# Kernel tuning notes

Measured on AMD Instinct MI355X. Metric: run time of the kernel, lower is better.

## Reference

```python
import jax, jax.numpy as jnp
import numpy as np

N = 50000      # nodes
E = 1600000    # edges (avg degree 32)
F_IN = 128     # num_features
DIM = 64       # hidden dim
L = 3          # num_gc_layers
G = 500        # graphs in batch


def setup_inputs() -> dict:
    key = jax.random.key(0)
    ks = jax.random.split(key, 16)
    inp = {}
    inp["x"] = jax.random.normal(ks[0], (N, F_IN), dtype=jnp.float32)
    inp["edge_index"] = jax.random.randint(ks[1], (2, E), 0, N, dtype=jnp.int32)
    inp["batch"] = jnp.sort(jax.random.randint(ks[2], (N,), 0, G, dtype=jnp.int32))
    # GIN layer MLP params: layer0 maps F_IN->DIM->DIM, later layers DIM->DIM->DIM
    d_in = F_IN
    ki = 3
    for i in range(L):
        inp[f"W1_{i}"] = jax.random.normal(ks[ki], (d_in, DIM), dtype=jnp.float32) / np.sqrt(d_in); ki += 1
        inp[f"b1_{i}"] = jnp.zeros((DIM,), dtype=jnp.float32)
        inp[f"W2_{i}"] = jax.random.normal(ks[ki], (DIM, DIM), dtype=jnp.float32) / np.sqrt(DIM); ki += 1
        inp[f"b2_{i}"] = jnp.zeros((DIM,), dtype=jnp.float32)
        d_in = DIM
    # final scoring head: concat readout -> dim * L inputs, 1 output
    inp["Wm"] = jax.random.normal(ks[ki], (DIM * L, 1), dtype=jnp.float32) / np.sqrt(DIM * L)
    inp["bm"] = jnp.zeros((1,), dtype=jnp.float32)
    return inp


def _segment_softmax(scores, seg, num_segments):
    # numerically stable softmax over elements grouped by seg; scores [M, 1]
    m = jax.ops.segment_max(scores, seg, num_segments=num_segments)
    e = jnp.exp(scores - m[seg])
    denom = jax.ops.segment_sum(e, seg, num_segments=num_segments)
    return e / denom[seg]


def _forward(x, edge_index, batch, params):
    src, dst = edge_index[0], edge_index[1]
    n = x.shape[0]
    xs = []
    h = x
    for i in range(L):
        W1, b1, W2, b2 = params[4 * i: 4 * i + 4]
        # GINConv (eps=0): h_i <- MLP(h_i + sum_{j->i} h_j)
        agg = jax.ops.segment_sum(h[src], dst, num_segments=n)
        h = jax.nn.relu((h + agg) @ W1 + b1) @ W2 + b2
        if i != L - 1:
            h = jax.nn.relu(h)
        xs.append(h)
    node_prob = jnp.concatenate(xs, axis=1)            # concat readout [N, DIM*L]
    Wm, bm = params[4 * L], params[4 * L + 1]
    node_score = node_prob @ Wm + bm                   # [N, 1]
    # lift_node_score_to_edge_score
    src_score = node_score[src]                        # [E, 1]
    dst_score = node_score[dst]
    edge_score = src_score * dst_score
    edge_prop = _segment_softmax(edge_score, dst, n)   # softmax over edges per dst
    new_score = jax.ops.segment_sum(src_score * edge_prop, dst, num_segments=n)
    node_score = node_score + new_score
    # final softmax over nodes grouped by graph id
    return _segment_softmax(node_score, batch, G)


def reference(x, edge_index, batch, W1_0, b1_0, W2_0, b2_0, W1_1, b1_1, W2_1, b2_1,
              W1_2, b1_2, W2_2, b2_2, Wm, bm):
    params = [W1_0, b1_0, W2_0, b2_0, W1_1, b1_1, W2_1, b2_1,
              W1_2, b1_2, W2_2, b2_2, Wm, bm]
    return _forward(x, edge_index, batch, params)
```

## Files before the change

### kernel.cpp

```cpp
#include <hip/hip_runtime.h>
#include <hip/hip_fp16.h>
#include <math.h>

#define N_NODES 50000
#define N_EDGES 1600000
#define N_GRAPH 500
#define CHUNKS 128
#define EPC (N_EDGES / CHUNKS)
#define NP1 (N_NODES + 1)
#define NIT ((EPC + 1023) / 1024)

__device__ __forceinline__ float rl(float v, int k) {
    return __int_as_float(__builtin_amdgcn_readlane(__float_as_int(v), k));
}
__device__ __forceinline__ void hacc(float4& a, uint2 w) {
    __half2 h01 = *reinterpret_cast<__half2*>(&w.x);
    __half2 h23 = *reinterpret_cast<__half2*>(&w.y);
    float2 f01 = __half22float2(h01);
    float2 f23 = __half22float2(h23);
    a.x += f01.x; a.y += f01.y; a.z += f23.x; a.w += f23.y;
}

__global__ __launch_bounds__(1024) void histsort_kernel(const int* __restrict__ src,
                                                        const int* __restrict__ dst,
                                                        int* __restrict__ csrc_chunk,
                                                        unsigned short* __restrict__ locs) {
    __shared__ unsigned packed[N_NODES / 2];
    __shared__ unsigned aux[1024];
    const int c = blockIdx.x;
    const int s0 = c * EPC;
    const int tid = threadIdx.x;

    for (int i = tid; i < N_NODES / 2; i += 1024) packed[i] = 0;
    __syncthreads();

    unsigned short lrv[NIT];
#pragma unroll
    for (int it = 0; it < NIT; it++) {
        int e = s0 + it * 1024 + tid;
        if (e < s0 + EPC) {
            int d = dst[e];
            int sh = (d & 1) * 16;
            unsigned old = atomicAdd(&packed[d >> 1], 1u << sh);
            lrv[it] = (unsigned short)((old >> sh) & 0xffffu);
        }
    }
    __syncthreads();

    const int W = 25;
    int w0 = tid * W;
    int w1 = min(w0 + W, N_NODES / 2);
    unsigned run = 0;
    for (int i = w0; i < w1; i++) {
        unsigned v = packed[i];
        unsigned lo = v & 0xffffu, hi = v >> 16;
        packed[i] = run | ((run + lo) << 16);
        run += lo + hi;
    }
    aux[tid] = run;
    __syncthreads();
    for (int off = 1; off < 1024; off <<= 1) {
        unsigned t = (tid >= off) ? aux[tid - off] : 0;
        __syncthreads();
        aux[tid] += t;
        __syncthreads();
    }
    unsigned b0 = (tid == 0) ? 0 : aux[tid - 1];
    if (b0) {
        unsigned addv = b0 | (b0 << 16);
        for (int i = w0; i < w1; i++) packed[i] += addv;
    }
    __syncthreads();

    int* outc = csrc_chunk + (size_t)c * EPC;
#pragma unroll
    for (int it = 0; it < NIT; it++) {
        int e = s0 + it * 1024 + tid;
        if (e < s0 + EPC) {
            int d = dst[e];
            unsigned pw = packed[d >> 1];
            unsigned loc = (d & 1) ? (pw >> 16) : (pw & 0xffffu);
            outc[loc + lrv[it]] = src[e];
        }
    }
    unsigned short* lc = locs + (size_t)c * NP1;
    for (int d = tid; d <= N_NODES; d += 1024) {
        unsigned short loc;
        if (d == N_NODES) {
            loc = (unsigned short)EPC;
        } else {
            unsigned pw = packed[d >> 1];
            loc = (unsigned short)((d & 1) ? (pw >> 16) : (pw & 0xffffu));
        }
        lc[d] = loc;
    }
}

__global__ __launch_bounds__(1024) void base_scan1_kernel(const unsigned short* __restrict__ locs,
                                                          unsigned short* __restrict__ base,
                                                          int* __restrict__ deg,
                                                          int* __restrict__ part, int N) {
    int d = blockIdx.x * 1024 + threadIdx.x;
    int run = 0;
    if (d < N) {
#pragma unroll 8
        for (int c = 0; c < CHUNKS; c++) {
            int l0 = locs[(size_t)c * NP1 + d];
            int l1 = locs[(size_t)c * NP1 + d + 1];
            base[(size_t)c * N + d] = (unsigned short)run;
            run += l1 - l0;
        }
        deg[d] = run;
    }
    int v = run;
#pragma unroll
    for (int o = 32; o >= 1; o >>= 1) v += __shfl_xor(v, o);
    __shared__ int red[16];
    if ((threadIdx.x & 63) == 0) red[threadIdx.x >> 6] = v;
    __syncthreads();
    if (threadIdx.x == 0) {
        int s = 0;
#pragma unroll
        for (int k = 0; k < 16; k++) s += red[k];
        part[blockIdx.x] = s;
    }
}

__global__ void scan2_kernel(int* __restrict__ part, int nb) {
    int lane = threadIdx.x;
    int v = (lane < nb) ? part[lane] : 0;
    int orig = v;
#pragma unroll
    for (int o = 1; o < 64; o <<= 1) {
        int t = __shfl_up(v, o);
        if (lane >= o) v += t;
    }
    if (lane < nb) part[lane] = v - orig;
    if (lane == nb - 1) part[nb] = v;
}

__global__ __launch_bounds__(1024) void scan3_kernel(const int* __restrict__ deg,
                                                     const int* __restrict__ part,
                                                     int* __restrict__ rowptr, int N) {
    int i = blockIdx.x * 1024 + threadIdx.x;
    int lane = threadIdx.x & 63;
    int w = threadIdx.x >> 6;
    int v = (i < N) ? deg[i] : 0;
    int inc = v;
#pragma unroll
    for (int o = 1; o < 64; o <<= 1) {
        int t = __shfl_up(inc, o);
        if (lane >= o) inc += t;
    }
    __shared__ int wsum[16];
    if (lane == 63) wsum[w] = inc;
    __syncthreads();
    if (threadIdx.x < 16) {
        int x = wsum[threadIdx.x];
        int xo = x;
#pragma unroll
        for (int o = 1; o < 16; o <<= 1) {
            int t = __shfl_up(x, o);
            if ((int)threadIdx.x >= o) x += t;
        }
        wsum[threadIdx.x] = x - xo;
    }
    __syncthreads();
    int b = part[blockIdx.x] + wsum[w];
    if (i < N) {
        rowptr[i] = b + inc - v;
        if (i == N - 1) rowptr[N] = b + inc;
    }
}

__global__ __launch_bounds__(256) void gatherfill_kernel(const int* __restrict__ csrc_chunk,
                                                         const unsigned short* __restrict__ locs,
                                                         const unsigned short* __restrict__ base,
                                                         const int* __restrict__ rowptr,
                                                         int* __restrict__ csr_src) {
    const int perXcd = N_NODES / 8;
    int xcd = blockIdx.x & 7;
    int idx = (blockIdx.x >> 3) * 4 + (threadIdx.x >> 6);
    if (idx >= perXcd) return;
    int wid = xcd * perXcd + idx;
    int lane = threadIdx.x & 63;
    int rp = rowptr[wid];
#pragma unroll
    for (int cc = 0; cc < 2; cc++) {
        int c = lane + cc * 64;
        const unsigned short* lc = locs + (size_t)c * NP1;
        int l0 = lc[wid];
        int l1 = lc[wid + 1];
        int cnt = l1 - l0;
        int ob = rp + (int)base[(size_t)c * N_NODES + wid];
        const int* in = csrc_chunk + (size_t)c * EPC + l0;
        for (int i = 0; i < cnt; i++) csr_src[ob + i] = in[i];
    }
}

__global__ __launch_bounds__(256) void agg_kernel(const __half* __restrict__ yh,
                                                  const int* __restrict__ rowptr,
                                                  const int* __restrict__ csr_src,
                                                  float* __restrict__ u, int N) {
    int wid = (blockIdx.x * 256 + threadIdx.x) >> 6;
    int lane = threadIdx.x & 63;
    if (wid >= N) return;
    int q = lane >> 4;
    int r = lane & 15;
    int start = rowptr[wid];
    int end = rowptr[wid + 1];
    float4 acc = make_float4(0.f, 0.f, 0.f, 0.f);
    int j = start;
    for (; j + 32 <= end; j += 32) {
        int s0 = csr_src[j + q];
        int s1 = csr_src[j + 4 + q];
        int s2 = csr_src[j + 8 + q];
        int s3 = csr_src[j + 12 + q];
        int s4 = csr_src[j + 16 + q];
        int s5 = csr_src[j + 20 + q];
        int s6 = csr_src[j + 24 + q];
        int s7 = csr_src[j + 28 + q];
        uint2 w0 = *(const uint2*)(yh + (size_t)s0 * 64 + r * 4);
        uint2 w1 = *(const uint2*)(yh + (size_t)s1 * 64 + r * 4);
        uint2 w2 = *(const uint2*)(yh + (size_t)s2 * 64 + r * 4);
        uint2 w3 = *(const uint2*)(yh + (size_t)s3 * 64 + r * 4);
        uint2 w4 = *(const uint2*)(yh + (size_t)s4 * 64 + r * 4);
        uint2 w5 = *(const uint2*)(yh + (size_t)s5 * 64 + r * 4);
        uint2 w6 = *(const uint2*)(yh + (size_t)s6 * 64 + r * 4);
        uint2 w7 = *(const uint2*)(yh + (size_t)s7 * 64 + r * 4);
        hacc(acc, w0); hacc(acc, w1); hacc(acc, w2); hacc(acc, w3);
        hacc(acc, w4); hacc(acc, w5); hacc(acc, w6); hacc(acc, w7);
    }
#pragma unroll
    for (int m = 0; m < 8; m++) {
        int e = j + 4 * m + q;
        if (e < end) {
            int s = csr_src[e];
            uint2 w = *(const uint2*)(yh + (size_t)s * 64 + r * 4);
            hacc(acc, w);
        }
    }
    acc.x += __shfl_xor(acc.x, 16);
    acc.y += __shfl_xor(acc.y, 16);
    acc.z += __shfl_xor(acc.z, 16);
    acc.w += __shfl_xor(acc.w, 16);
    acc.x += __shfl_xor(acc.x, 32);
    acc.y += __shfl_xor(acc.y, 32);
    acc.z += __shfl_xor(acc.z, 32);
    acc.w += __shfl_xor(acc.w, 32);
    if (lane < 16) {
        uint2 w = *(const uint2*)(yh + (size_t)wid * 64 + r * 4);
        hacc(acc, w);
        *(float4*)(u + (size_t)wid * 64 + r * 4) = acc;
    }
}

__global__ __launch_bounds__(256) void gemm0_kernel(const float* __restrict__ x,
                                                    const float* __restrict__ W1,
                                                    __half* __restrict__ y0,
                                                    int N, int totalWaves) {
    int lane = threadIdx.x & 63;
    int wid = (blockIdx.x * 256 + threadIdx.x) >> 6;
    float wA[64], wB[64];
#pragma unroll
    for (int k = 0; k < 64; k++) wA[k] = W1[k * 64 + lane];
#pragma unroll
    for (int k = 0; k < 64; k++) wB[k] = W1[(64 + k) * 64 + lane];
    for (int node = wid; node < N; node += totalWaves) {
        float xa = x[(size_t)node * 128 + lane];
        float xb = x[(size_t)node * 128 + 64 + lane];
        float a0 = 0.f, a1 = 0.f, a2 = 0.f, a3 = 0.f;
#pragma unroll
        for (int k = 0; k < 64; k += 4) {
            a0 = fmaf(rl(xa, k + 0), wA[k + 0], a0);
            a1 = fmaf(rl(xa, k + 1), wA[k + 1], a1);
            a2 = fmaf(rl(xa, k + 2), wA[k + 2], a2);
            a3 = fmaf(rl(xa, k + 3), wA[k + 3], a3);
        }
#pragma unroll
        for (int k = 0; k < 64; k += 4) {
            a0 = fmaf(rl(xb, k + 0), wB[k + 0], a0);
            a1 = fmaf(rl(xb, k + 1), wB[k + 1], a1);
            a2 = fmaf(rl(xb, k + 2), wB[k + 2], a2);
            a3 = fmaf(rl(xb, k + 3), wB[k + 3], a3);
        }
        y0[(size_t)node * 64 + lane] = __float2half((a0 + a1) + (a2 + a3));
    }
}

template <int LAYER>
__global__ __launch_bounds__(256) void mlpAB_kernel(const float* __restrict__ u,
                                                    const float* __restrict__ b1,
                                                    const float* __restrict__ W2,
                                                    const float* __restrict__ b2,
                                                    const float* __restrict__ W1n,
                                                    const float* __restrict__ Wm,
                                                    __half* __restrict__ ynext,
                                                    float* __restrict__ score,
                                                    int N, int totalWaves) {
    int lane = threadIdx.x & 63;
    int wid = (blockIdx.x * 256 + threadIdx.x) >> 6;
    float w2[64], w1[64];
#pragma unroll
    for (int k = 0; k < 64; k++) w2[k] = W2[k * 64 + lane];
#pragma unroll
    for (int k = 0; k < 64; k++) w1[k] = W1n[k * 64 + lane];
    float bb1 = b1[lane], bb2 = b2[lane], wm = Wm[LAYER * 64 + lane];

    int node = wid;
    float uin = (node < N) ? u[(size_t)node * 64 + lane] : 0.f;
    for (; node < N; node += totalWaves) {
        int nn = node + totalWaves;
        float unext = (nn < N) ? u[(size_t)nn * 64 + lane] : 0.f;
        float t = fmaxf(uin + bb1, 0.f);
        float a0 = 0.f, a1 = 0.f, a2 = 0.f, a3 = 0.f;
#pragma unroll
        for (int k = 0; k < 64; k += 4) {
            a0 = fmaf(rl(t, k + 0), w2[k + 0], a0);
            a1 = fmaf(rl(t, k + 1), w2[k + 1], a1);
            a2 = fmaf(rl(t, k + 2), w2[k + 2], a2);
            a3 = fmaf(rl(t, k + 3), w2[k + 3], a3);
        }
        float h = fmaxf(bb2 + ((a0 + a1) + (a2 + a3)), 0.f);
        float p = h * wm;
#pragma unroll
        for (int o = 32; o >= 1; o >>= 1) p += __shfl_xor(p, o);
        if (lane == 0) {
            if (LAYER == 0) score[node] = p;
            else score[node] += p;
        }
        float y0 = 0.f, y1 = 0.f, y2 = 0.f, y3 = 0.f;
#pragma unroll
        for (int k = 0; k < 64; k += 4) {
            y0 = fmaf(rl(h, k + 0), w1[k + 0], y0);
            y1 = fmaf(rl(h, k + 1), w1[k + 1], y1);
            y2 = fmaf(rl(h, k + 2), w1[k + 2], y2);
            y3 = fmaf(rl(h, k + 3), w1[k + 3], y3);
        }
        ynext[(size_t)node * 64 + lane] = __float2half((y0 + y1) + (y2 + y3));
        uin = unext;
    }
}

__global__ __launch_bounds__(256) void mlpA2_kernel(const float* __restrict__ u,
                                                    const float* __restrict__ b1,
                                                    const float* __restrict__ W2,
                                                    const float* __restrict__ b2,
                                                    const float* __restrict__ Wm,
                                                    float* __restrict__ score,
                                                    int N, int totalWaves) {
    int lane = threadIdx.x & 63;
    int wid = (blockIdx.x * 256 + threadIdx.x) >> 6;
    float w2[64];
#pragma unroll
    for (int k = 0; k < 64; k++) w2[k] = W2[k * 64 + lane];
    float bb1 = b1[lane], bb2 = b2[lane], wm = Wm[2 * 64 + lane];

    int node = wid;
    float uin = (node < N) ? u[(size_t)node * 64 + lane] : 0.f;
    for (; node < N; node += totalWaves) {
        int nn = node + totalWaves;
        float unext = (nn < N) ? u[(size_t)nn * 64 + lane] : 0.f;
        float t = fmaxf(uin + bb1, 0.f);
        float a0 = 0.f, a1 = 0.f, a2 = 0.f, a3 = 0.f;
#pragma unroll
        for (int k = 0; k < 64; k += 4) {
            a0 = fmaf(rl(t, k + 0), w2[k + 0], a0);
            a1 = fmaf(rl(t, k + 1), w2[k + 1], a1);
            a2 = fmaf(rl(t, k + 2), w2[k + 2], a2);
            a3 = fmaf(rl(t, k + 3), w2[k + 3], a3);
        }
        float h = bb2 + ((a0 + a1) + (a2 + a3));
        float p = h * wm;
#pragma unroll
        for (int o = 32; o >= 1; o >>= 1) p += __shfl_xor(p, o);
        if (lane == 0) score[node] += p;
        uin = unext;
    }
}

__global__ __launch_bounds__(256) void edge_softmax_kernel(const float* __restrict__ score,
                                                           const int* __restrict__ rowptr,
                                                           const int* __restrict__ csr_src,
                                                           const float* __restrict__ bm,
                                                           float* __restrict__ nsf, int N) {
    int wid = (blockIdx.x * blockDim.x + threadIdx.x) >> 6;
    int lane = threadIdx.x & 63;
    if (wid >= N) return;
    float b = bm[0];
    float sd = score[wid] + b;
    int start = rowptr[wid];
    int end = rowptr[wid + 1];
    bool has0 = (start + lane < end);
    float ss0 = 0.f;
    float m = -INFINITY;
    if (has0) {
        ss0 = score[csr_src[start + lane]] + b;
        m = ss0 * sd;
    }
    for (int j = start + 64 + lane; j < end; j += 64) {
        float ss = score[csr_src[j]] + b;
        m = fmaxf(m, ss * sd);
    }
#pragma unroll
    for (int o = 32; o >= 1; o >>= 1) m = fmaxf(m, __shfl_xor(m, o));
    float se = 0.f, swe = 0.f;
    if (m > -INFINITY) {
        if (has0) {
            float e0 = expf(ss0 * sd - m);
            se += e0;
            swe += ss0 * e0;
        }
        for (int j = start + 64 + lane; j < end; j += 64) {
            float ss = score[csr_src[j]] + b;
            float e = expf(ss * sd - m);
            se += e;
            swe += ss * e;
        }
#pragma unroll
        for (int o = 32; o >= 1; o >>= 1) {
            se += __shfl_xor(se, o);
            swe += __shfl_xor(swe, o);
        }
    }
    float ns = (se > 0.f) ? (swe / se) : 0.f;
    if (lane == 0) nsf[wid] = sd + ns;
}

__global__ __launch_bounds__(256) void graph_softmax_kernel(const float* __restrict__ nsf,
                                                            const int* __restrict__ batch,
                                                            float* __restrict__ out, int N) {
    int g = blockIdx.x;
    int tid = threadIdx.x;
    int lo = 0, hi = N;
    while (lo < hi) { int mid = (lo + hi) >> 1; if (batch[mid] < g) lo = mid + 1; else hi = mid; }
    int s0 = lo;
    hi = N;
    while (lo < hi) { int mid = (lo + hi) >> 1; if (batch[mid] < g + 1) lo = mid + 1; else hi = mid; }
    int s1 = lo;

    __shared__ float red[4];
    __shared__ float bval;
    float m = -INFINITY;
    for (int i = s0 + tid; i < s1; i += 256) m = fmaxf(m, nsf[i]);
#pragma unroll
    for (int o = 32; o >= 1; o >>= 1) m = fmaxf(m, __shfl_xor(m, o));
    if ((tid & 63) == 0) red[tid >> 6] = m;
    __syncthreads();
    if (tid == 0) bval = fmaxf(fmaxf(red[0], red[1]), fmaxf(red[2], red[3]));
    __syncthreads();
    float bmx = bval;
    float s = 0.f;
    for (int i = s0 + tid; i < s1; i += 256) {
        float e = expf(nsf[i] - bmx);
        out[i] = e;
        s += e;
    }
#pragma unroll
    for (int o = 32; o >= 1; o >>= 1) s += __shfl_xor(s, o);
    __syncthreads();
    if ((tid & 63) == 0) red[tid >> 6] = s;
    __syncthreads();
    if (tid == 0) bval = red[0] + red[1] + red[2] + red[3];
    __syncthreads();
    float inv = 1.f / bval;
    for (int i = s0 + tid; i < s1; i += 256) out[i] *= inv;
}

extern "C" void kernel_launch(void* const* d_in, const int* in_sizes, int n_in,
                              void* d_out, int out_size, void* d_ws, size_t ws_size,
                              hipStream_t stream) {
    const int N = N_NODES, E = N_EDGES;

    const float* x = (const float*)d_in[0];
    const int* ei = (const int*)d_in[1];
    const int* batch = (const int*)d_in[2];
    const float* W1a[3] = {(const float*)d_in[3], (const float*)d_in[7], (const float*)d_in[11]};
    const float* b1a[3] = {(const float*)d_in[4], (const float*)d_in[8], (const float*)d_in[12]};
    const float* W2a[3] = {(const float*)d_in[5], (const float*)d_in[9], (const float*)d_in[13]};
    const float* b2a[3] = {(const float*)d_in[6], (const float*)d_in[10], (const float*)d_in[14]};
    const float* Wm = (const float*)d_in[15];
    const float* bm = (const float*)d_in[16];
    float* out = (float*)d_out;

    const int* srcp = ei;
    const int* dstp = ei + E;

    float* ubuf = (float*)d_ws;
    int* csrc_chunk = (int*)ubuf;
    __half* yA = (__half*)(ubuf + (size_t)N * 64);
    __half* yB = yA + (size_t)N * 64;
    float* score = (float*)(yB + (size_t)N * 64);
    float* nsf = score + N;
    int* deg = (int*)(nsf + N);
    int* rowptr = deg + N;
    int* part = rowptr + N + 1;
    int* csr_src = part + 64;
    unsigned short* locs = (unsigned short*)(csr_src + E);
    unsigned short* base = locs + (size_t)CHUNKS * NP1;

    histsort_kernel<<<CHUNKS, 1024, 0, stream>>>(srcp, dstp, csrc_chunk, locs);

    const int nbScan = (N + 1023) / 1024;
    base_scan1_kernel<<<nbScan, 1024, 0, stream>>>(locs, base, deg, part, N);
    scan2_kernel<<<1, 64, 0, stream>>>(part, nbScan);
    scan3_kernel<<<nbScan, 1024, 0, stream>>>(deg, part, rowptr, N);

    const int gfBlocks = 8 * ((N / 8 + 3) / 4);
    gatherfill_kernel<<<gfBlocks, 256, 0, stream>>>(csrc_chunk, locs, base, rowptr, csr_src);

    const int gw = 4096;
    gemm0_kernel<<<1024, 256, 0, stream>>>(x, W1a[0], yA, N, gw);

    int aggBlocks = (N + 3) / 4;

    agg_kernel<<<aggBlocks, 256, 0, stream>>>(yA, rowptr, csr_src, ubuf, N);
    mlpAB_kernel<0><<<1024, 256, 0, stream>>>(ubuf, b1a[0], W2a[0], b2a[0], W1a[1], Wm, yB, score, N, gw);

    agg_kernel<<<aggBlocks, 256, 0, stream>>>(yB, rowptr, csr_src, ubuf, N);
    mlpAB_kernel<1><<<1024, 256, 0, stream>>>(ubuf, b1a[1], W2a[1], b2a[1], W1a[2], Wm, yA, score, N, gw);

    agg_kernel<<<aggBlocks, 256, 0, stream>>>(yA, rowptr, csr_src, ubuf, N);
    mlpA2_kernel<<<1024, 256, 0, stream>>>(ubuf, b1a[2], W2a[2], b2a[2], Wm, score, N, gw);

    edge_softmax_kernel<<<(N + 3) / 4, 256, 0, stream>>>(score, rowptr, csr_src, bm, nsf, N);

    graph_softmax_kernel<<<N_GRAPH, 256, 0, stream>>>(nsf, batch, out, N);
}
```

Before: 339.4 us.

## Fuse first-layer GEMM into histogram kernel and widen aggregation gathers to 16 bytes

Merges the layer-0 feature GEMM into the histogram-sort launch as extra blocks. The histogram runs on only 128 blocks, so the GEMM can use the otherwise idle compute units, and one launch is removed. The fused GEMM keeps half of W1 in registers and reads the other half from the shared-memory array the histogram path also uses, to respect register limits at 1024 threads. Separately, the aggregation kernel now loads 8 halves per lane with 16-byte gathers and covers 8 edges per pass instead of 4, which halves the number of lanes per row. This adds more shuffle reductions and raises register pressure.

```diff
diff --git a/kernel.cpp b/kernel.cpp
--- a/kernel.cpp
+++ b/kernel.cpp
@@ -9,90 +9,128 @@
 #define EPC (N_EDGES / CHUNKS)
 #define NP1 (N_NODES + 1)
 #define NIT ((EPC + 1023) / 1024)
+#define GEMM_BLOCKS 128
 
 __device__ __forceinline__ float rl(float v, int k) {
     return __int_as_float(__builtin_amdgcn_readlane(__float_as_int(v), k));
 }
-__device__ __forceinline__ void hacc(float4& a, uint2 w) {
-    __half2 h01 = *reinterpret_cast<__half2*>(&w.x);
-    __half2 h23 = *reinterpret_cast<__half2*>(&w.y);
-    float2 f01 = __half22float2(h01);
-    float2 f23 = __half22float2(h23);
-    a.x += f01.x; a.y += f01.y; a.z += f23.x; a.w += f23.y;
-}
-
-__global__ __launch_bounds__(1024) void histsort_kernel(const int* __restrict__ src,
-                                                        const int* __restrict__ dst,
-                                                        int* __restrict__ csrc_chunk,
-                                                        unsigned short* __restrict__ locs) {
+__device__ __forceinline__ void hacc16(float4& A, float4& B, uint4 w) {
+    float2 f0 = __half22float2(*reinterpret_cast<__half2*>(&w.x));
+    float2 f1 = __half22float2(*reinterpret_cast<__half2*>(&w.y));
+    float2 f2 = __half22float2(*reinterpret_cast<__half2*>(&w.z));
+    float2 f3 = __half22float2(*reinterpret_cast<__half2*>(&w.w));
+    A.x += f0.x; A.y += f0.y; A.z += f1.x; A.w += f1.y;
+    B.x += f2.x; B.y += f2.y; B.z += f3.x; B.w += f3.y;
+}
+
+__global__ __launch_bounds__(1024) void hist_gemm0_kernel(const int* __restrict__ src,
+                                                          const int* __restrict__ dst,
+                                                          int* __restrict__ csrc_chunk,
+                                                          unsigned short* __restrict__ locs,
+                                                          const float* __restrict__ x,
+                                                          const float* __restrict__ W1,
+                                                          __half* __restrict__ y0, int N) {
     __shared__ unsigned packed[N_NODES / 2];
     __shared__ unsigned aux[1024];
-    const int c = blockIdx.x;
-    const int s0 = c * EPC;
     const int tid = threadIdx.x;
 
-    for (int i = tid; i < N_NODES / 2; i += 1024) packed[i] = 0;
-    __syncthreads();
-
-    unsigned short lrv[NIT];
-#pragma unroll
-    for (int it = 0; it < NIT; it++) {
-        int e = s0 + it * 1024 + tid;
-        if (e < s0 + EPC) {
-            int d = dst[e];
-            int sh = (d & 1) * 16;
-            unsigned old = atomicAdd(&packed[d >> 1], 1u << sh);
-            lrv[it] = (unsigned short)((old >> sh) & 0xffffu);
-        }
-    }
-    __syncthreads();
-
-    const int W = 25;
-    int w0 = tid * W;
-    int w1 = min(w0 + W, N_NODES / 2);
-    unsigned run = 0;
-    for (int i = w0; i < w1; i++) {
-        unsigned v = packed[i];
-        unsigned lo = v & 0xffffu, hi = v >> 16;
-        packed[i] = run | ((run + lo) << 16);
-        run += lo + hi;
-    }
-    aux[tid] = run;
-    __syncthreads();
-    for (int off = 1; off < 1024; off <<= 1) {
-        unsigned t = (tid >= off) ? aux[tid - off] : 0;
+    if (blockIdx.x < CHUNKS) {
+        const int c = blockIdx.x;
+        const int s0 = c * EPC;
+
+        for (int i = tid; i < N_NODES / 2; i += 1024) packed[i] = 0;
         __syncthreads();
-        aux[tid] += t;
+
+        unsigned short lrv[NIT];
+#pragma unroll
+        for (int it = 0; it < NIT; it++) {
+            int e = s0 + it * 1024 + tid;
+            if (e < s0 + EPC) {
+                int d = dst[e];
+                int sh = (d & 1) * 16;
+                unsigned old = atomicAdd(&packed[d >> 1], 1u << sh);
+                lrv[it] = (unsigned short)((old >> sh) & 0xffffu);
+            }
+        }
         __syncthreads();
-    }
-    unsigned b0 = (tid == 0) ? 0 : aux[tid - 1];
-    if (b0) {
-        unsigned addv = b0 | (b0 << 16);
-        for (int i = w0; i < w1; i++) packed[i] += addv;
-    }
-    __syncthreads();
-
-    int* outc = csrc_chunk + (size_t)c * EPC;
-#pragma unroll
-    for (int it = 0; it < NIT; it++) {
-        int e = s0 + it * 1024 + tid;
-        if (e < s0 + EPC) {
-            int d = dst[e];
-            unsigned pw = packed[d >> 1];
-            unsigned loc = (d & 1) ? (pw >> 16) : (pw & 0xffffu);
-            outc[loc + lrv[it]] = src[e];
-        }
-    }
-    unsigned short* lc = locs + (size_t)c * NP1;
-    for (int d = tid; d <= N_NODES; d += 1024) {
-        unsigned short loc;
-        if (d == N_NODES) {
-            loc = (unsigned short)EPC;
-        } else {
-            unsigned pw = packed[d >> 1];
-            loc = (unsigned short)((d & 1) ? (pw >> 16) : (pw & 0xffffu));
-        }
-        lc[d] = loc;
+
+        const int W = 25;
+        int w0 = tid * W;
+        int w1 = min(w0 + W, N_NODES / 2);
+        unsigned run = 0;
+        for (int i = w0; i < w1; i++) {
+            unsigned v = packed[i];
+            unsigned lo = v & 0xffffu, hi = v >> 16;
+            packed[i] = run | ((run + lo) << 16);
+            run += lo + hi;
+        }
+        aux[tid] = run;
+        __syncthreads();
+        for (int off = 1; off < 1024; off <<= 1) {
+            unsigned t = (tid >= off) ? aux[tid - off] : 0;
+            __syncthreads();
+            aux[tid] += t;
+            __syncthreads();
+        }
+        unsigned b0 = (tid == 0) ? 0 : aux[tid - 1];
+        if (b0) {
+            unsigned addv = b0 | (b0 << 16);
+            for (int i = w0; i < w1; i++) packed[i] += addv;
+        }
+        __syncthreads();
+
+        int* outc = csrc_chunk + (size_t)c * EPC;
+#pragma unroll
+        for (int it = 0; it < NIT; it++) {
+            int e = s0 + it * 1024 + tid;
+            if (e < s0 + EPC) {
+                int d = dst[e];
+                unsigned pw = packed[d >> 1];
+                unsigned loc = (d & 1) ? (pw >> 16) : (pw & 0xffffu);
+                outc[loc + lrv[it]] = src[e];
+            }
+        }
+        unsigned short* lc = locs + (size_t)c * NP1;
+        for (int d = tid; d <= N_NODES; d += 1024) {
+            unsigned short loc;
+            if (d == N_NODES) {
+                loc = (unsigned short)EPC;
+            } else {
+                unsigned pw = packed[d >> 1];
+                loc = (unsigned short)((d & 1) ? (pw >> 16) : (pw & 0xffffu));
+            }
+            lc[d] = loc;
+        }
+    } else {
+        float* sW = (float*)packed;
+        for (int i = tid; i < 64 * 64; i += 1024) sW[i] = W1[64 * 64 + i];
+        __syncthreads();
+        int lane = tid & 63;
+        float w[64];
+#pragma unroll
+        for (int k = 0; k < 64; k++) w[k] = W1[k * 64 + lane];
+        int wid = ((blockIdx.x - CHUNKS) * 1024 + tid) >> 6;
+        const int totalWaves = GEMM_BLOCKS * 16;
+        for (int node = wid; node < N; node += totalWaves) {
+            float xa = x[(size_t)node * 128 + lane];
+            float xb = x[(size_t)node * 128 + 64 + lane];
+            float a0 = 0.f, a1 = 0.f, a2 = 0.f, a3 = 0.f;
+#pragma unroll
+            for (int k = 0; k < 64; k += 4) {
+                a0 = fmaf(rl(xa, k + 0), w[k + 0], a0);
+                a1 = fmaf(rl(xa, k + 1), w[k + 1], a1);
+                a2 = fmaf(rl(xa, k + 2), w[k + 2], a2);
+                a3 = fmaf(rl(xa, k + 3), w[k + 3], a3);
+            }
+#pragma unroll
+            for (int k = 0; k < 64; k += 4) {
+                a0 = fmaf(rl(xb, k + 0), sW[(k + 0) * 64 + lane], a0);
+                a1 = fmaf(rl(xb, k + 1), sW[(k + 1) * 64 + lane], a1);
+                a2 = fmaf(rl(xb, k + 2), sW[(k + 2) * 64 + lane], a2);
+                a3 = fmaf(rl(xb, k + 3), sW[(k + 3) * 64 + lane], a3);
+            }
+            y0[(size_t)node * 64 + lane] = __float2half((a0 + a1) + (a2 + a3));
+        }
     }
 }
 
@@ -205,86 +243,54 @@
     int wid = (blockIdx.x * 256 + threadIdx.x) >> 6;
     int lane = threadIdx.x & 63;
     if (wid >= N) return;
-    int q = lane >> 4;
-    int r = lane & 15;
+    int q = lane >> 3;
+    int r = lane & 7;
     int start = rowptr[wid];
     int end = rowptr[wid + 1];
-    float4 acc = make_float4(0.f, 0.f, 0.f, 0.f);
+    float4 A = make_float4(0.f, 0.f, 0.f, 0.f);
+    float4 B = make_float4(0.f, 0.f, 0.f, 0.f);
     int j = start;
-    for (; j + 32 <= end; j += 32) {
+    for (; j + 64 <= end; j += 64) {
         int s0 = csr_src[j + q];
-        int s1 = csr_src[j + 4 + q];
-        int s2 = csr_src[j + 8 + q];
-        int s3 = csr_src[j + 12 + q];
-        int s4 = csr_src[j + 16 + q];
-        int s5 = csr_src[j + 20 + q];
-        int s6 = csr_src[j + 24 + q];
-        int s7 = csr_src[j + 28 + q];
-        uint2 w0 = *(const uint2*)(yh + (size_t)s0 * 64 + r * 4);
-        uint2 w1 = *(const uint2*)(yh + (size_t)s1 * 64 + r * 4);
-        uint2 w2 = *(const uint2*)(yh + (size_t)s2 * 64 + r * 4);
-        uint2 w3 = *(const uint2*)(yh + (size_t)s3 * 64 + r * 4);
-        uint2 w4 = *(const uint2*)(yh + (size_t)s4 * 64 + r * 4);
-        uint2 w5 = *(const uint2*)(yh + (size_t)s5 * 64 + r * 4);
-        uint2 w6 = *(const uint2*)(yh + (size_t)s6 * 64 + r * 4);
-        uint2 w7 = *(const uint2*)(yh + (size_t)s7 * 64 + r * 4);
-        hacc(acc, w0); hacc(acc, w1); hacc(acc, w2); hacc(acc, w3);
-        hacc(acc, w4); hacc(acc, w5); hacc(acc, w6); hacc(acc, w7);
+        int s1 = csr_src[j + 8 + q];
+        int s2 = csr_src[j + 16 + q];
+        int s3 = csr_src[j + 24 + q];
+        int s4 = csr_src[j + 32 + q];
+        int s5 = csr_src[j + 40 + q];
+        int s6 = csr_src[j + 48 + q];
+        int s7 = csr_src[j + 56 + q];
+        uint4 w0 = *(const uint4*)(yh + (size_t)s0 * 64 + r * 8);
+        uint4 w1 = *(const uint4*)(yh + (size_t)s1 * 64 + r * 8);
+        uint4 w2 = *(const uint4*)(yh + (size_t)s2 * 64 + r * 8);
+        uint4 w3 = *(const uint4*)(yh + (size_t)s3 * 64 + r * 8);
+        uint4 w4 = *(const uint4*)(yh + (size_t)s4 * 64 + r * 8);
+        uint4 w5 = *(const uint4*)(yh + (size_t)s5 * 64 + r * 8);
+        uint4 w6 = *(const uint4*)(yh + (size_t)s6 * 64 + r * 8);
+        uint4 w7 = *(const uint4*)(yh + (size_t)s7 * 64 + r * 8);
+        hacc16(A, B, w0); hacc16(A, B, w1); hacc16(A, B, w2); hacc16(A, B, w3);
+        hacc16(A, B, w4); hacc16(A, B, w5); hacc16(A, B, w6); hacc16(A, B, w7);
     }
 #pragma unroll
     for (int m = 0; m < 8; m++) {
-        int e = j + 4 * m + q;
+        int e = j + 8 * m + q;
         if (e < end) {
             int s = csr_src[e];
-            uint2 w = *(const uint2*)(yh + (size_t)s * 64 + r * 4);
-            hacc(acc, w);
-        }
-    }
-    acc.x += __shfl_xor(acc.x, 16);
-    acc.y += __shfl_xor(acc.y, 16);
-    acc.z += __shfl_xor(acc.z, 16);
-    acc.w += __shfl_xor(acc.w, 16);
-    acc.x += __shfl_xor(acc.x, 32);
-    acc.y += __shfl_xor(acc.y, 32);
-    acc.z += __shfl_xor(acc.z, 32);
-    acc.w += __shfl_xor(acc.w, 32);
-    if (lane < 16) {
-        uint2 w = *(const uint2*)(yh + (size_t)wid * 64 + r * 4);
-        hacc(acc, w);
-        *(float4*)(u + (size_t)wid * 64 + r * 4) = acc;
-    }
-}
-
-__global__ __launch_bounds__(256) void gemm0_kernel(const float* __restrict__ x,
-                                                    const float* __restrict__ W1,
-                                                    __half* __restrict__ y0,
-                                                    int N, int totalWaves) {
-    int lane = threadIdx.x & 63;
-    int wid = (blockIdx.x * 256 + threadIdx.x) >> 6;
-    float wA[64], wB[64];
-#pragma unroll
-    for (int k = 0; k < 64; k++) wA[k] = W1[k * 64 + lane];
-#pragma unroll
-    for (int k = 0; k < 64; k++) wB[k] = W1[(64 + k) * 64 + lane];
-    for (int node = wid; node < N; node += totalWaves) {
-        float xa = x[(size_t)node * 128 + lane];
-        float xb = x[(size_t)node * 128 + 64 + lane];
-        float a0 = 0.f, a1 = 0.f, a2 = 0.f, a3 = 0.f;
-#pragma unroll
-        for (int k = 0; k < 64; k += 4) {
-            a0 = fmaf(rl(xa, k + 0), wA[k + 0], a0);
-            a1 = fmaf(rl(xa, k + 1), wA[k + 1], a1);
-            a2 = fmaf(rl(xa, k + 2), wA[k + 2], a2);
-            a3 = fmaf(rl(xa, k + 3), wA[k + 3], a3);
-        }
-#pragma unroll
-        for (int k = 0; k < 64; k += 4) {
-            a0 = fmaf(rl(xb, k + 0), wB[k + 0], a0);
-            a1 = fmaf(rl(xb, k + 1), wB[k + 1], a1);
-            a2 = fmaf(rl(xb, k + 2), wB[k + 2], a2);
-            a3 = fmaf(rl(xb, k + 3), wB[k + 3], a3);
-        }
-        y0[(size_t)node * 64 + lane] = __float2half((a0 + a1) + (a2 + a3));
+            uint4 w = *(const uint4*)(yh + (size_t)s * 64 + r * 8);
+            hacc16(A, B, w);
+        }
+    }
+#pragma unroll
+    for (int o = 8; o <= 32; o <<= 1) {
+        A.x += __shfl_xor(A.x, o); A.y += __shfl_xor(A.y, o);
+        A.z += __shfl_xor(A.z, o); A.w += __shfl_xor(A.w, o);
+        B.x += __shfl_xor(B.x, o); B.y += __shfl_xor(B.y, o);
+        B.z += __shfl_xor(B.z, o); B.w += __shfl_xor(B.w, o);
+    }
+    if (lane < 8) {
+        uint4 w = *(const uint4*)(yh + (size_t)wid * 64 + r * 8);
+        hacc16(A, B, w);
+        *(float4*)(u + (size_t)wid * 64 + r * 8) = A;
+        *(float4*)(u + (size_t)wid * 64 + r * 8 + 4) = B;
     }
 }
 
@@ -499,7 +505,8 @@
     unsigned short* locs = (unsigned short*)(csr_src + E);
     unsigned short* base = locs + (size_t)CHUNKS * NP1;
 
-    histsort_kernel<<<CHUNKS, 1024, 0, stream>>>(srcp, dstp, csrc_chunk, locs);
+    hist_gemm0_kernel<<<CHUNKS + GEMM_BLOCKS, 1024, 0, stream>>>(srcp, dstp, csrc_chunk, locs,
+                                                                 x, W1a[0], yA, N);
 
     const int nbScan = (N + 1023) / 1024;
     base_scan1_kernel<<<nbScan, 1024, 0, stream>>>(locs, base, deg, part, N);
@@ -510,8 +517,6 @@
     gatherfill_kernel<<<gfBlocks, 256, 0, stream>>>(csrc_chunk, locs, base, rowptr, csr_src);
 
     const int gw = 4096;
-    gemm0_kernel<<<1024, 256, 0, stream>>>(x, W1a[0], yA, N, gw);
-
     int aggBlocks = (N + 3) / 4;
 
     agg_kernel<<<aggBlocks, 256, 0, stream>>>(yA, rowptr, csr_src, ubuf, N);
```

New measurement: 372.5 us. +9.8%, slower.
